# Optimization experiments

Measured on AMD Instinct MI355X. Metric: run time of the kernel, lower is better.

## Reference

```python
import jax, jax.numpy as jnp
import numpy as np

N_NODES = 50000


def gcn_layer(x, src, dst, ew, W, b, n_nodes):
    # PyG GCNConv: add self-loops (weight 1), symmetric deg^-1/2 normalization,
    # linear transform, scatter-add aggregation at destination, then bias.
    loop = jnp.arange(n_nodes, dtype=src.dtype)
    s = jnp.concatenate([src, loop])
    d = jnp.concatenate([dst, loop])
    w = jnp.concatenate([ew, jnp.ones((n_nodes,), dtype=ew.dtype)])
    deg = jax.ops.segment_sum(w, d, num_segments=n_nodes)  # [N]
    dinv = jnp.where(deg > 0, jax.lax.rsqrt(jnp.where(deg > 0, deg, 1.0)), 0.0)
    norm = dinv[s] * w * dinv[d]  # [E+N]
    h = x @ W  # [N, out]
    msg = h[s] * norm[:, None]  # gather + scale, [E+N, out]
    out = jax.ops.segment_sum(msg, d, num_segments=n_nodes)  # scatter-add
    return out + b


def setup_inputs() -> dict:
    key = jax.random.key(0)
    k1, k2, k3, k4, k5, k6, k7 = jax.random.split(key, 7)
    N, E, C_IN, C_OUT = N_NODES, 600000, 128, 128
    x = jax.random.normal(k1, (N, C_IN), dtype=jnp.float32)
    edge_index = jax.random.randint(k2, (2, E), 0, N, dtype=jnp.int64)
    edge_weight = jax.random.uniform(k3, (E,), dtype=jnp.float32)
    # Glorot-style init like PyG's Linear default
    s1 = 1.0 / np.sqrt(C_IN)
    s2 = 1.0 / np.sqrt(C_OUT)
    W1 = jax.random.uniform(k4, (C_IN, C_OUT), jnp.float32, -s1, s1)
    b1 = jnp.zeros((C_OUT,), dtype=jnp.float32)
    W2 = jax.random.uniform(k5, (C_OUT, C_OUT), jnp.float32, -s2, s2)
    b2 = jnp.zeros((C_OUT,), dtype=jnp.float32)
    return {"x": x, "edge_index": edge_index, "edge_weight": edge_weight,
            "W1": W1, "b1": b1, "W2": W2, "b2": b2}


def reference(x, edge_index, edge_weight, W1, b1, W2, b2):
    src, dst = edge_index[0], edge_index[1]
    h = jax.nn.relu(gcn_layer(x, src, dst, edge_weight, W1, b1, N_NODES))
    return jax.nn.relu(gcn_layer(h, src, dst, edge_weight, W2, b2, N_NODES))
```

## Files before the change

### kernel.cpp

```cpp
#include <hip/hip_runtime.h>
#include <math.h>

#define CH   128
#define CH4  32
#define TPB  256
#define SCANB 1024
#define WIMG 16384
#define NREP 8

typedef __attribute__((ext_vector_type(8))) short short8;
typedef __attribute__((ext_vector_type(4))) float floatx4;

static __device__ __forceinline__ unsigned short f2bf(float f) {
    unsigned u = __float_as_uint(f);
    return (unsigned short)((u + 0x7fffu + ((u >> 16) & 1u)) >> 16);
}
static __device__ __forceinline__ float bf2f(unsigned short s) {
    return __uint_as_float(((unsigned)s) << 16);
}
static __device__ __forceinline__ float4 bf4_to_f4(ushort4 u) {
    return make_float4(bf2f(u.x), bf2f(u.y), bf2f(u.z), bf2f(u.w));
}

__global__ void k_prep(const float* __restrict__ W1, const float* __restrict__ W2,
                       short* __restrict__ Wsplit) {
    int i = blockIdx.x * blockDim.x + threadIdx.x;
    if (i >= 2 * CH * CH) return;
    int layer = i >> 14;
    int idx   = i & 16383;
    int k = idx >> 7, c = idx & 127;
    float w = (layer ? W2 : W1)[k * CH + c];
    unsigned short hi = f2bf(w);
    unsigned short lo = f2bf(w - bf2f(hi));
    int colh = c >> 6, nn = c & 63;
    int kt = k >> 5, q = (k & 31) >> 3, j = k & 7;
    int ns = nn >> 4, ln = q * 16 + (nn & 15);
    size_t base = (size_t)(layer * 2 + colh) * WIMG;
    size_t off  = ((size_t)(kt * 4 + ns) * 64 + ln) * 8 + j;
    Wsplit[base + off]        = (short)hi;
    Wsplit[base + 8192 + off] = (short)lo;
}

static __device__ __forceinline__ void gemm_body_f32(
        const float* __restrict__ X, const short* __restrict__ Wfrag,
        unsigned short* __restrict__ H, int n, int tile, int colh, int tid) {
    __shared__ __align__(16) short sW[2][4][4][64][8];
    {
        const float4* gsrc = (const float4*)Wfrag;
        float4* ldst = (float4*)sW;
        #pragma unroll
        for (int i = 0; i < 8; ++i)
            ldst[i * TPB + tid] = gsrc[i * TPB + tid];
    }
    __syncthreads();

    const int lane = tid & 63;
    const int wv   = tid >> 6;
    const int q    = lane >> 4;
    const int m    = lane & 15;
    const int row0 = tile * 64 + wv * 16;
    if (row0 >= n) return;

    int rrow = row0 + m;
    if (rrow > n - 1) rrow = n - 1;

    const float4* xr = (const float4*)(X + (size_t)rrow * CH);
    float4 xa[4][2];
    #pragma unroll
    for (int kt = 0; kt < 4; ++kt) {
        xa[kt][0] = xr[kt * 8 + q * 2 + 0];
        xa[kt][1] = xr[kt * 8 + q * 2 + 1];
    }

    floatx4 acc[4];
    #pragma unroll
    for (int ns = 0; ns < 4; ++ns) acc[ns] = (floatx4){0.f, 0.f, 0.f, 0.f};

    #pragma unroll
    for (int kt = 0; kt < 4; ++kt) {
        float xf[8] = { xa[kt][0].x, xa[kt][0].y, xa[kt][0].z, xa[kt][0].w,
                        xa[kt][1].x, xa[kt][1].y, xa[kt][1].z, xa[kt][1].w };
        short8 ah, al;
        #pragma unroll
        for (int j = 0; j < 8; ++j) {
            float v = xf[j];
            unsigned short h = f2bf(v);
            ah[j] = (short)h;
            al[j] = (short)f2bf(v - bf2f(h));
        }
        #pragma unroll
        for (int ns = 0; ns < 4; ++ns) {
            short8 bh = *(const short8*)&sW[0][kt][ns][lane][0];
            short8 bl = *(const short8*)&sW[1][kt][ns][lane][0];
            acc[ns] = __builtin_amdgcn_mfma_f32_16x16x32_bf16(ah, bh, acc[ns], 0, 0, 0);
            acc[ns] = __builtin_amdgcn_mfma_f32_16x16x32_bf16(al, bh, acc[ns], 0, 0, 0);
            acc[ns] = __builtin_amdgcn_mfma_f32_16x16x32_bf16(ah, bl, acc[ns], 0, 0, 0);
        }
    }

    #pragma unroll
    for (int ns = 0; ns < 4; ++ns) {
        #pragma unroll
        for (int reg = 0; reg < 4; ++reg) {
            int r = row0 + q * 4 + reg;
            if (r < n)
                H[(size_t)r * CH + colh * 64 + ns * 16 + m] = f2bf(acc[ns][reg]);
        }
    }
}

__global__ __launch_bounds__(TPB, 4)
void k_gemm_rank(const float* __restrict__ X, const short* __restrict__ Wsplit,
                 unsigned short* __restrict__ H, int n,
                 const int* __restrict__ dst, int* __restrict__ counts_rep,
                 int* __restrict__ rank, int E, int nbE, int Np) {
    int bx = blockIdx.x;
    if (bx < nbE) {
        int e = bx * TPB + threadIdx.x;
        if (e < E) {
            int d = dst[e];
            if ((unsigned)d < (unsigned)n) {
                int rep = e & (NREP - 1);
                rank[e] = atomicAdd(&counts_rep[rep * Np + d], 1);
            }
        }
    } else {
        bx -= nbE;
        int colh = bx & 1;
        gemm_body_f32(X, Wsplit + (size_t)colh * WIMG, H, n, bx >> 1, colh,
                      threadIdx.x);
    }
}

__global__ __launch_bounds__(TPB, 4)
void k_gemm_bf(const unsigned short* __restrict__ X, const short* __restrict__ Wsplit,
               unsigned short* __restrict__ H, int n) {
    __shared__ __align__(16) short sW[4][4][64][8];
    const int tid  = threadIdx.x;
    const int colh = (int)blockIdx.x & 1;
    const int tile = (int)blockIdx.x >> 1;
    {
        const float4* gsrc = (const float4*)(Wsplit + (size_t)colh * WIMG);
        float4* ldst = (float4*)sW;
        #pragma unroll
        for (int i = 0; i < 4; ++i)
            ldst[i * TPB + tid] = gsrc[i * TPB + tid];
    }
    __syncthreads();

    const int lane = tid & 63;
    const int wv   = tid >> 6;
    const int q    = lane >> 4;
    const int m    = lane & 15;
    const int row0 = tile * 64 + wv * 16;
    if (row0 >= n) return;

    int rrow = row0 + m;
    if (rrow > n - 1) rrow = n - 1;

    const short8* xr8 = (const short8*)(X + (size_t)rrow * CH);
    short8 a[4];
    #pragma unroll
    for (int kt = 0; kt < 4; ++kt) a[kt] = xr8[kt * 4 + q];

    floatx4 acc[4];
    #pragma unroll
    for (int ns = 0; ns < 4; ++ns) acc[ns] = (floatx4){0.f, 0.f, 0.f, 0.f};

    #pragma unroll
    for (int kt = 0; kt < 4; ++kt) {
        #pragma unroll
        for (int ns = 0; ns < 4; ++ns) {
            short8 bh = *(const short8*)&sW[kt][ns][lane][0];
            acc[ns] = __builtin_amdgcn_mfma_f32_16x16x32_bf16(a[kt], bh, acc[ns], 0, 0, 0);
        }
    }

    #pragma unroll
    for (int ns = 0; ns < 4; ++ns) {
        #pragma unroll
        for (int reg = 0; reg < 4; ++reg) {
            int r = row0 + q * 4 + reg;
            if (r < n)
                H[(size_t)r * CH + colh * 64 + ns * 16 + m] = f2bf(acc[ns][reg]);
        }
    }
}

__global__ __launch_bounds__(SCANB)
void k_scan1(const int* __restrict__ counts_rep, int Np,
             int* __restrict__ counts_tot, int* __restrict__ repoff8,
             int* __restrict__ row_start, int* __restrict__ partials,
             int* __restrict__ pp_s, int* __restrict__ done, int nb, int n) {
    __shared__ int s[SCANB];
    __shared__ int slast;
    int gid = blockIdx.x * SCANB + threadIdx.x;
    int c[NREP];
    int v = 0;
    #pragma unroll
    for (int r = 0; r < NREP; ++r) {
        c[r] = (gid < n) ? counts_rep[r * Np + gid] : 0;
        v += c[r];
    }
    s[threadIdx.x] = v;
    __syncthreads();
    for (int off = 1; off < SCANB; off <<= 1) {
        int t = (threadIdx.x >= off) ? s[threadIdx.x - off] : 0;
        __syncthreads();
        s[threadIdx.x] += t;
        __syncthreads();
    }
    if (gid < n) {
        row_start[gid]  = s[threadIdx.x] - v;
        counts_tot[gid] = v;
        int pre = 0;
        int ro[NREP];
        #pragma unroll
        for (int r = 0; r < NREP; ++r) { ro[r] = pre; pre += c[r]; }
        ((int4*)repoff8)[gid * 2 + 0] = make_int4(ro[0], ro[1], ro[2], ro[3]);
        ((int4*)repoff8)[gid * 2 + 1] = make_int4(ro[4], ro[5], ro[6], ro[7]);
    }
    if (threadIdx.x == SCANB - 1) {
        partials[blockIdx.x] = s[SCANB - 1];
        __threadfence();
        int old = atomicAdd(done, 1);
        slast = (old == nb - 1);
    }
    __syncthreads();
    if (slast && threadIdx.x < 64) {
        int pv = (threadIdx.x < nb) ? atomicAdd(&partials[threadIdx.x], 0) : 0;
        int inc = pv;
        #pragma unroll
        for (int off = 1; off < 64; off <<= 1) {
            int t = __shfl_up(inc, off, 64);
            if ((threadIdx.x & 63) >= off) inc += t;
        }
        if (threadIdx.x < nb) pp_s[threadIdx.x] = inc - pv;
    }
}

__global__ void k_fill(const int* __restrict__ src, const int* __restrict__ dst,
                       const float* __restrict__ ew, const int* __restrict__ row_start,
                       const int* __restrict__ pp_s, const int* __restrict__ repoff8,
                       const int* __restrict__ rank, int2* __restrict__ edges,
                       int E, int n) {
    int e = blockIdx.x * blockDim.x + threadIdx.x;
    if (e >= E) return;
    int s = src[e], d = dst[e];
    if ((unsigned)s >= (unsigned)n || (unsigned)d >= (unsigned)n) return;
    int rep = e & (NREP - 1);
    int base = row_start[d] + pp_s[d >> 10] + repoff8[d * NREP + rep];
    edges[base + rank[e]] = make_int2(s, __float_as_int(ew[e]));
}

__global__ void k_deg(const int* __restrict__ row_start, const int* __restrict__ pp_s,
                      const int* __restrict__ counts, const int2* __restrict__ edges,
                      float* __restrict__ dinv, int n) {
    int i = blockIdx.x * blockDim.x + threadIdx.x;
    if (i >= n) return;
    int j = row_start[i] + pp_s[i >> 10], end = j + counts[i];
    float sum = 1.0f;
    for (; j < end; ++j) sum += __int_as_float(edges[j].y);
    dinv[i] = rsqrtf(sum);
}

template<int FIXUP>
static __device__ __forceinline__ float4 agg_node(
        const ushort4* __restrict__ h4, int2* __restrict__ edges,
        const float* __restrict__ dinv, const float4 b, int node, int tx,
        const int* __restrict__ row_start, const int* __restrict__ pp_s,
        const int* __restrict__ counts) {
    float di = dinv[node];
    float4 hv = bf4_to_f4(h4[(size_t)node * CH4 + tx]);
    float4 acc = make_float4(0.f, 0.f, 0.f, 0.f);
    int j   = row_start[node] + pp_s[node >> 10];
    int end = j + counts[node];

    for (; j + 8 <= end; j += 8) {
        int2 e[8];
        #pragma unroll
        for (int i = 0; i < 8; ++i) e[i] = edges[j + i];
        ushort4 g[8];
        #pragma unroll
        for (int i = 0; i < 8; ++i) g[i] = h4[(size_t)e[i].x * CH4 + tx];
        float w[8];
        #pragma unroll
        for (int i = 0; i < 8; ++i) {
            w[i] = __int_as_float(e[i].y);
            if (FIXUP) w[i] *= dinv[e[i].x];
        }
        if (FIXUP && tx == 0) {
            #pragma unroll
            for (int i = 0; i < 8; ++i) edges[j + i].y = __float_as_int(w[i]);
        }
        #pragma unroll
        for (int i = 0; i < 8; ++i) {
            float4 gf = bf4_to_f4(g[i]);
            acc.x += gf.x * w[i]; acc.y += gf.y * w[i];
            acc.z += gf.z * w[i]; acc.w += gf.w * w[i];
        }
    }
    if (j + 4 <= end) {
        int2 e[4];
        #pragma unroll
        for (int i = 0; i < 4; ++i) e[i] = edges[j + i];
        ushort4 g[4];
        #pragma unroll
        for (int i = 0; i < 4; ++i) g[i] = h4[(size_t)e[i].x * CH4 + tx];
        float w[4];
        #pragma unroll
        for (int i = 0; i < 4; ++i) {
            w[i] = __int_as_float(e[i].y);
            if (FIXUP) w[i] *= dinv[e[i].x];
        }
        if (FIXUP && tx == 0) {
            #pragma unroll
            for (int i = 0; i < 4; ++i) edges[j + i].y = __float_as_int(w[i]);
        }
        #pragma unroll
        for (int i = 0; i < 4; ++i) {
            float4 gf = bf4_to_f4(g[i]);
            acc.x += gf.x * w[i]; acc.y += gf.y * w[i];
            acc.z += gf.z * w[i]; acc.w += gf.w * w[i];
        }
        j += 4;
    }
    for (; j < end; ++j) {
        int2 e0 = edges[j];
        float w0 = __int_as_float(e0.y);
        if (FIXUP) w0 *= dinv[e0.x];
        if (FIXUP && tx == 0) edges[j].y = __float_as_int(w0);
        float4 gf = bf4_to_f4(h4[(size_t)e0.x * CH4 + tx]);
        acc.x += gf.x * w0; acc.y += gf.y * w0;
        acc.z += gf.z * w0; acc.w += gf.w * w0;
    }

    float sc = di * di;
    return make_float4(hv.x * sc + b.x + di * acc.x,
                       hv.y * sc + b.y + di * acc.y,
                       hv.z * sc + b.z + di * acc.z,
                       hv.w * sc + b.w + di * acc.w);
}

__global__ __launch_bounds__(TPB)
void k_aggregate1(const unsigned short* __restrict__ h,
                  const int* __restrict__ row_start, const int* __restrict__ pp_s,
                  const int* __restrict__ counts, int2* __restrict__ edges,
                  const float* __restrict__ dinv, const float* __restrict__ bias,
                  unsigned short* __restrict__ out, int n) {
    int t = blockIdx.x * blockDim.x + threadIdx.x;
    int node = t >> 5;
    if (node >= n) return;
    int tx = t & 31;
    const float4 b = ((const float4*)bias)[tx];
    float4 o = agg_node<1>((const ushort4*)h, edges, dinv, b, node, tx,
                           row_start, pp_s, counts);
    ushort4 u = make_ushort4(f2bf(fmaxf(o.x, 0.f)), f2bf(fmaxf(o.y, 0.f)),
                             f2bf(fmaxf(o.z, 0.f)), f2bf(fmaxf(o.w, 0.f)));
    ((ushort4*)out)[(size_t)node * CH4 + tx] = u;
}

__global__ __launch_bounds__(TPB)
void k_aggregate2(const unsigned short* __restrict__ h,
                  const int* __restrict__ row_start, const int* __restrict__ pp_s,
                  const int* __restrict__ counts, int2* __restrict__ edges,
                  const float* __restrict__ dinv, const float* __restrict__ bias,
                  float* __restrict__ out, int n) {
    int t = blockIdx.x * blockDim.x + threadIdx.x;
    int node = t >> 5;
    if (node >= n) return;
    int tx = t & 31;
    const float4 b = ((const float4*)bias)[tx];
    float4 o = agg_node<0>((const ushort4*)h, edges, dinv, b, node, tx,
                           row_start, pp_s, counts);
    o.x = fmaxf(o.x, 0.f); o.y = fmaxf(o.y, 0.f);
    o.z = fmaxf(o.z, 0.f); o.w = fmaxf(o.w, 0.f);
    ((float4*)out)[(size_t)node * CH4 + tx] = o;
}

extern "C" void kernel_launch(void* const* d_in, const int* in_sizes, int n_in,
                              void* d_out, int out_size, void* d_ws, size_t ws_size,
                              hipStream_t stream) {
    const float* x  = (const float*)d_in[0];
    const int*   ei = (const int*)d_in[1];
    const float* ew = (const float*)d_in[2];
    const float* W1 = (const float*)d_in[3];
    const float* b1 = (const float*)d_in[4];
    const float* W2 = (const float*)d_in[5];
    const float* b2 = (const float*)d_in[6];
    float* out = (float*)d_out;

    const int N = in_sizes[0] / CH;
    const int E = in_sizes[2];
    const int* src = ei;
    const int* dst = ei + E;

    size_t Np = ((size_t)N + 255) & ~(size_t)255;
    size_t Ep = ((size_t)E + 63) & ~(size_t)63;
    float* ws          = (float*)d_ws;
    float* dinv        = ws;
    unsigned short* h  = (unsigned short*)(dinv + Np);
    unsigned short* o1 = h + (size_t)N * CH;
    unsigned short* h2 = o1 + (size_t)N * CH;
    int*   counts_rep  = (int*)(h2 + (size_t)N * CH);
    int*   done        = counts_rep + NREP * Np;
    size_t zero_bytes  = (size_t)NREP * Np * 4 + 256;
    int*  counts_tot   = done + 64;
    int*  row_start    = counts_tot + Np;
    int*  repoff8      = row_start + Np;
    int*  rank         = repoff8 + NREP * Np;
    int*  partials     = rank + Ep;
    int*  pp_s         = partials + 64;
    int2* edges        = (int2*)(pp_s + 64);
    short* Wsplit      = (short*)(edges + E);

    const int nbN    = (N + TPB - 1) / TPB;
    const int nbE    = (E + TPB - 1) / TPB;
    const int nbAgg  = (int)(((size_t)N * 32 + TPB - 1) / TPB);
    const int nbScan = (N + SCANB - 1) / SCANB;
    const int nbGemm2 = 2 * ((N + 63) / 64);
    const int nbPrep  = (2 * CH * CH + TPB - 1) / TPB;

    hipMemsetAsync(counts_rep, 0, zero_bytes, stream);
    k_prep     <<<nbPrep, TPB, 0, stream>>>(W1, W2, Wsplit);

    k_gemm_rank<<<nbE + nbGemm2, TPB, 0, stream>>>(x, Wsplit, h, N, dst,
                                                   counts_rep, rank, E, nbE, (int)Np);
    k_scan1    <<<nbScan, SCANB, 0, stream>>>(counts_rep, (int)Np, counts_tot,
                                              repoff8, row_start, partials,
                                              pp_s, done, nbScan, N);
    k_fill     <<<nbE, TPB, 0, stream>>>(src, dst, ew, row_start, pp_s, repoff8,
                                         rank, edges, E, N);
    k_deg      <<<nbN, TPB, 0, stream>>>(row_start, pp_s, counts_tot, edges,
                                         dinv, N);

    k_aggregate1<<<nbAgg, TPB, 0, stream>>>(h, row_start, pp_s, counts_tot,
                                            edges, dinv, b1, o1, N);
    k_gemm_bf   <<<nbGemm2, TPB, 0, stream>>>(o1, Wsplit + 2 * (size_t)WIMG, h2, N);
    k_aggregate2<<<nbAgg, TPB, 0, stream>>>(h2, row_start, pp_s, counts_tot,
                                            edges, dinv, b2, out, N);
}
```

Measured before the change: 228.5 us.

## Widen aggregation to 16 lanes per node with 16-byte bf16 gathers

The aggregation kernels now assign 16 threads per node, each handling 8 channels through a 16-byte short8 gather, instead of 32 threads each loading 8 bytes. This halves the number of load instructions and the redundant edge-list reads per node, at the cost of more registers per thread and fewer threads per node in flight. Separately, the edge ranking part of the fused gemm/rank kernel now processes 4 edges per thread with a grid stride, cutting the number of ranking blocks.

Measured after the change: 215.7 us. 1.06x faster.

```diff
diff --git a/kernel.cpp b/kernel.cpp
--- a/kernel.cpp
+++ b/kernel.cpp
@@ -10,6 +10,7 @@
 
 typedef __attribute__((ext_vector_type(8))) short short8;
 typedef __attribute__((ext_vector_type(4))) float floatx4;
+typedef __attribute__((ext_vector_type(8))) float float8;
 
 static __device__ __forceinline__ unsigned short f2bf(float f) {
     unsigned u = __float_as_uint(f);
@@ -18,8 +19,11 @@
 static __device__ __forceinline__ float bf2f(unsigned short s) {
     return __uint_as_float(((unsigned)s) << 16);
 }
-static __device__ __forceinline__ float4 bf4_to_f4(ushort4 u) {
-    return make_float4(bf2f(u.x), bf2f(u.y), bf2f(u.z), bf2f(u.w));
+static __device__ __forceinline__ float8 bf8_to_f8(short8 u) {
+    float8 f;
+    #pragma unroll
+    for (int i = 0; i < 8; ++i) f[i] = bf2f((unsigned short)u[i]);
+    return f;
 }
 
 __global__ void k_prep(const float* __restrict__ W1, const float* __restrict__ W2,
@@ -113,19 +117,23 @@
 void k_gemm_rank(const float* __restrict__ X, const short* __restrict__ Wsplit,
                  unsigned short* __restrict__ H, int n,
                  const int* __restrict__ dst, int* __restrict__ counts_rep,
-                 int* __restrict__ rank, int E, int nbE, int Np) {
+                 int* __restrict__ rank, int E, int nbE4, int Np) {
     int bx = blockIdx.x;
-    if (bx < nbE) {
+    if (bx < nbE4) {
+        int stride = nbE4 * TPB;
         int e = bx * TPB + threadIdx.x;
-        if (e < E) {
-            int d = dst[e];
-            if ((unsigned)d < (unsigned)n) {
-                int rep = e & (NREP - 1);
-                rank[e] = atomicAdd(&counts_rep[rep * Np + d], 1);
+        #pragma unroll
+        for (int it = 0; it < 4; ++it, e += stride) {
+            if (e < E) {
+                int d = dst[e];
+                if ((unsigned)d < (unsigned)n) {
+                    int rep = e & (NREP - 1);
+                    rank[e] = atomicAdd(&counts_rep[rep * Np + d], 1);
+                }
             }
         }
     } else {
-        bx -= nbE;
+        bx -= nbE4;
         int colh = bx & 1;
         gemm_body_f32(X, Wsplit + (size_t)colh * WIMG, H, n, bx >> 1, colh,
                       threadIdx.x);
@@ -265,14 +273,17 @@
 }
 
 template<int FIXUP>
-static __device__ __forceinline__ float4 agg_node(
-        const ushort4* __restrict__ h4, int2* __restrict__ edges,
-        const float* __restrict__ dinv, const float4 b, int node, int tx,
+static __device__ __forceinline__ float8 agg_node8(
+        const short8* __restrict__ h8, int2* __restrict__ edges,
+        const float* __restrict__ dinv, const float8 b, int node, int tx,
         const int* __restrict__ row_start, const int* __restrict__ pp_s,
         const int* __restrict__ counts) {
     float di = dinv[node];
-    float4 hv = bf4_to_f4(h4[(size_t)node * CH4 + tx]);
-    float4 acc = make_float4(0.f, 0.f, 0.f, 0.f);
+    float8 hv = bf8_to_f8(h8[(size_t)node * 16 + tx]);
+    float8 acc;
+    #pragma unroll
+    for (int i = 0; i < 8; ++i) acc[i] = 0.f;
+
     int j   = row_start[node] + pp_s[node >> 10];
     int end = j + counts[node];
 
@@ -280,9 +291,9 @@
         int2 e[8];
         #pragma unroll
         for (int i = 0; i < 8; ++i) e[i] = edges[j + i];
-        ushort4 g[8];
-        #pragma unroll
-        for (int i = 0; i < 8; ++i) g[i] = h4[(size_t)e[i].x * CH4 + tx];
+        short8 g[8];
+        #pragma unroll
+        for (int i = 0; i < 8; ++i) g[i] = h8[(size_t)e[i].x * 16 + tx];
         float w[8];
         #pragma unroll
         for (int i = 0; i < 8; ++i) {
@@ -295,18 +306,18 @@
         }
         #pragma unroll
         for (int i = 0; i < 8; ++i) {
-            float4 gf = bf4_to_f4(g[i]);
-            acc.x += gf.x * w[i]; acc.y += gf.y * w[i];
-            acc.z += gf.z * w[i]; acc.w += gf.w * w[i];
+            float8 gf = bf8_to_f8(g[i]);
+            #pragma unroll
+            for (int c = 0; c < 8; ++c) acc[c] += gf[c] * w[i];
         }
     }
     if (j + 4 <= end) {
         int2 e[4];
         #pragma unroll
         for (int i = 0; i < 4; ++i) e[i] = edges[j + i];
-        ushort4 g[4];
-        #pragma unroll
-        for (int i = 0; i < 4; ++i) g[i] = h4[(size_t)e[i].x * CH4 + tx];
+        short8 g[4];
+        #pragma unroll
+        for (int i = 0; i < 4; ++i) g[i] = h8[(size_t)e[i].x * 16 + tx];
         float w[4];
         #pragma unroll
         for (int i = 0; i < 4; ++i) {
@@ -319,9 +330,9 @@
         }
         #pragma unroll
         for (int i = 0; i < 4; ++i) {
-            float4 gf = bf4_to_f4(g[i]);
-            acc.x += gf.x * w[i]; acc.y += gf.y * w[i];
-            acc.z += gf.z * w[i]; acc.w += gf.w * w[i];
+            float8 gf = bf8_to_f8(g[i]);
+            #pragma unroll
+            for (int c = 0; c < 8; ++c) acc[c] += gf[c] * w[i];
         }
         j += 4;
     }
@@ -330,16 +341,16 @@
         float w0 = __int_as_float(e0.y);
         if (FIXUP) w0 *= dinv[e0.x];
         if (FIXUP && tx == 0) edges[j].y = __float_as_int(w0);
-        float4 gf = bf4_to_f4(h4[(size_t)e0.x * CH4 + tx]);
-        acc.x += gf.x * w0; acc.y += gf.y * w0;
-        acc.z += gf.z * w0; acc.w += gf.w * w0;
+        float8 gf = bf8_to_f8(h8[(size_t)e0.x * 16 + tx]);
+        #pragma unroll
+        for (int c = 0; c < 8; ++c) acc[c] += gf[c] * w0;
     }
 
     float sc = di * di;
-    return make_float4(hv.x * sc + b.x + di * acc.x,
-                       hv.y * sc + b.y + di * acc.y,
-                       hv.z * sc + b.z + di * acc.z,
-                       hv.w * sc + b.w + di * acc.w);
+    float8 o;
+    #pragma unroll
+    for (int c = 0; c < 8; ++c) o[c] = hv[c] * sc + b[c] + di * acc[c];
+    return o;
 }
 
 __global__ __launch_bounds__(TPB)
@@ -349,15 +360,18 @@
                   const float* __restrict__ dinv, const float* __restrict__ bias,
                   unsigned short* __restrict__ out, int n) {
     int t = blockIdx.x * blockDim.x + threadIdx.x;
-    int node = t >> 5;
+    int node = t >> 4;
     if (node >= n) return;
-    int tx = t & 31;
-    const float4 b = ((const float4*)bias)[tx];
-    float4 o = agg_node<1>((const ushort4*)h, edges, dinv, b, node, tx,
-                           row_start, pp_s, counts);
-    ushort4 u = make_ushort4(f2bf(fmaxf(o.x, 0.f)), f2bf(fmaxf(o.y, 0.f)),
-                             f2bf(fmaxf(o.z, 0.f)), f2bf(fmaxf(o.w, 0.f)));
-    ((ushort4*)out)[(size_t)node * CH4 + tx] = u;
+    int tx = t & 15;
+    float8 b;
+    #pragma unroll
+    for (int c = 0; c < 8; ++c) b[c] = bias[tx * 8 + c];
+    float8 o = agg_node8<1>((const short8*)h, edges, dinv, b, node, tx,
+                            row_start, pp_s, counts);
+    short8 u;
+    #pragma unroll
+    for (int c = 0; c < 8; ++c) u[c] = (short)f2bf(fmaxf(o[c], 0.f));
+    ((short8*)out)[(size_t)node * 16 + tx] = u;
 }
 
 __global__ __launch_bounds__(TPB)
@@ -367,15 +381,20 @@
                   const float* __restrict__ dinv, const float* __restrict__ bias,
                   float* __restrict__ out, int n) {
     int t = blockIdx.x * blockDim.x + threadIdx.x;
-    int node = t >> 5;
+    int node = t >> 4;
     if (node >= n) return;
-    int tx = t & 31;
-    const float4 b = ((const float4*)bias)[tx];
-    float4 o = agg_node<0>((const ushort4*)h, edges, dinv, b, node, tx,
-                           row_start, pp_s, counts);
-    o.x = fmaxf(o.x, 0.f); o.y = fmaxf(o.y, 0.f);
-    o.z = fmaxf(o.z, 0.f); o.w = fmaxf(o.w, 0.f);
-    ((float4*)out)[(size_t)node * CH4 + tx] = o;
+    int tx = t & 15;
+    float8 b;
+    #pragma unroll
+    for (int c = 0; c < 8; ++c) b[c] = bias[tx * 8 + c];
+    float8 o = agg_node8<0>((const short8*)h, edges, dinv, b, node, tx,
+                            row_start, pp_s, counts);
+    float4 lo = make_float4(fmaxf(o[0], 0.f), fmaxf(o[1], 0.f),
+                            fmaxf(o[2], 0.f), fmaxf(o[3], 0.f));
+    float4 hi = make_float4(fmaxf(o[4], 0.f), fmaxf(o[5], 0.f),
+                            fmaxf(o[6], 0.f), fmaxf(o[7], 0.f));
+    ((float4*)out)[(size_t)node * CH4 + tx * 2 + 0] = lo;
+    ((float4*)out)[(size_t)node * CH4 + tx * 2 + 1] = hi;
 }
 
 extern "C" void kernel_launch(void* const* d_in, const int* in_sizes, int n_in,
@@ -416,7 +435,8 @@
 
     const int nbN    = (N + TPB - 1) / TPB;
     const int nbE    = (E + TPB - 1) / TPB;
-    const int nbAgg  = (int)(((size_t)N * 32 + TPB - 1) / TPB);
+    const int nbE4   = (E + TPB * 4 - 1) / (TPB * 4);
+    const int nbAgg  = (int)(((size_t)N * 16 + TPB - 1) / TPB);
     const int nbScan = (N + SCANB - 1) / SCANB;
     const int nbGemm2 = 2 * ((N + 63) / 64);
     const int nbPrep  = (2 * CH * CH + TPB - 1) / TPB;
@@ -424,8 +444,8 @@
     hipMemsetAsync(counts_rep, 0, zero_bytes, stream);
     k_prep     <<<nbPrep, TPB, 0, stream>>>(W1, W2, Wsplit);
 
-    k_gemm_rank<<<nbE + nbGemm2, TPB, 0, stream>>>(x, Wsplit, h, N, dst,
-                                                   counts_rep, rank, E, nbE, (int)Np);
+    k_gemm_rank<<<nbE4 + nbGemm2, TPB, 0, stream>>>(x, Wsplit, h, N, dst,
+                                                    counts_rep, rank, E, nbE4, (int)Np);
     k_scan1    <<<nbScan, SCANB, 0, stream>>>(counts_rep, (int)Np, counts_tot,
                                               repoff8, row_start, partials,
                                               pp_s, done, nbScan, N);
```
